# Performance work log

Measured on AMD Instinct MI355X. Metric: run time of the kernel, lower is better.

The kernel has to match this reference:

```python
import jax, jax.numpy as jnp
import numpy as np

POOL = 7          # output pooling resolution (Mask R-CNN box head)
IMG = 1024.0      # assumed input image size (boxes are normalized)
CANON = 224.0     # canonical ROI size for FPN level assignment


def _make_boxes(key, B, N):
    k1, k2, k3, k4 = jax.random.split(key, 4)
    y1 = jax.random.uniform(k1, (B, N)) * 0.7
    x1 = jax.random.uniform(k2, (B, N)) * 0.7
    h = jax.random.uniform(k3, (B, N)) * 0.28 + 0.01
    w = jax.random.uniform(k4, (B, N)) * 0.28 + 0.01
    return jnp.stack([y1, x1, jnp.minimum(y1 + h, 1.0), jnp.minimum(x1 + w, 1.0)], axis=-1)


def setup_inputs() -> dict:
    key = jax.random.key(0)
    k3, k4, k5, k6, kb = jax.random.split(key, 5)
    B, C, N = 2, 256, 1000
    return {
        "p3": jax.random.normal(k3, (B, 128, 128, C), jnp.float32),
        "p4": jax.random.normal(k4, (B, 64, 64, C), jnp.float32),
        "p5": jax.random.normal(k5, (B, 32, 32, C), jnp.float32),
        "p6": jax.random.normal(k6, (B, 16, 16, C), jnp.float32),
        "proposals": _make_boxes(kb, B, N),
    }


def _crop_resize(f, boxes):
    # f: [H, W, C]; boxes: [N, 4] normalized (y1, x1, y2, x2).
    # Matches tf.image.crop_and_resize bilinear sampling (crop_size > 1).
    H, W, _ = f.shape
    y1, x1, y2, x2 = boxes[:, 0], boxes[:, 1], boxes[:, 2], boxes[:, 3]
    t = jnp.arange(POOL, dtype=f.dtype) / (POOL - 1)          # [P]
    ys = (y1[:, None] + t[None, :] * (y2 - y1)[:, None]) * (H - 1)  # [N, P]
    xs = (x1[:, None] + t[None, :] * (x2 - x1)[:, None]) * (W - 1)  # [N, P]
    y0f = jnp.floor(ys); x0f = jnp.floor(xs)
    fy = ys - y0f; fx = xs - x0f                                # fractional parts
    y0 = jnp.clip(y0f.astype(jnp.int32), 0, H - 1)
    y1i = jnp.clip(y0 + 1, 0, H - 1)
    x0 = jnp.clip(x0f.astype(jnp.int32), 0, W - 1)
    x1i = jnp.clip(x0 + 1, 0, W - 1)
    # gather 4 corners: index broadcast [N,P,1] x [N,1,P] -> [N,P,P,C]
    v00 = f[y0[:, :, None], x0[:, None, :]]
    v01 = f[y0[:, :, None], x1i[:, None, :]]
    v10 = f[y1i[:, :, None], x0[:, None, :]]
    v11 = f[y1i[:, :, None], x1i[:, None, :]]
    wy = fy[:, :, None, None]; wx = fx[:, None, :, None]
    top = v00 + wx * (v01 - v00)
    bot = v10 + wx * (v11 - v10)
    return top + wy * (bot - top)                               # [N, P, P, C]


def reference(p3, p4, p5, p6, proposals):
    # proposals: [B, N, 4] normalized (y1, x1, y2, x2)
    h = proposals[..., 2] - proposals[..., 0]
    w = proposals[..., 3] - proposals[..., 1]
    # FPN level assignment (levels 3..6)
    roi_level = jnp.log2(jnp.sqrt(jnp.maximum(h * w, 0.0)) / (CANON / IMG) + 1e-8)
    lvl = jnp.clip(4 + jnp.round(roi_level).astype(jnp.int32), 3, 6)  # [B, N]
    B, N = lvl.shape
    C = p3.shape[-1]
    pooled = jnp.zeros((B, N, POOL, POOL, C), p3.dtype)
    for li, f in zip((3, 4, 5, 6), (p3, p4, p5, p6)):
        p = jax.vmap(_crop_resize)(f, proposals)                # [B, N, P, P, C]
        pooled = jnp.where((lvl == li)[:, :, None, None, None], p, pooled)
    return pooled
```

## Files before the change

### kernel.cpp

```cpp
#include <hip/hip_runtime.h>

#define POOL 7
#define NPTS 49

typedef float f4 __attribute__((ext_vector_type(4)));

__device__ __forceinline__ f4 ld4(const float* p) { return *(const f4*)p; }

__device__ __forceinline__ int roi_level(float dy, float dx) {
    const float rl = log2f(sqrtf(fmaxf(dy * dx, 0.0f)) / 0.21875f + 1e-8f);
    int lvl = 4 + (int)rintf(rl);
    return lvl < 3 ? 3 : (lvl > 6 ? 6 : lvl);
}

__device__ __forceinline__ int bucket_key(const float* props, int r, int N) {
    const f4 p = ld4(props + (size_t)r * 4);
    const int lvl = roi_level(p.z - p.x, p.w - p.y);
    const float yc = 0.5f * (p.x + p.z);
    int oct = (int)(yc * 8.0f);
    oct = oct < 0 ? 0 : (oct > 7 ? 7 : oct);
    int lg = lvl - 3; lg = lg < 0 ? 0 : (lg > 1 ? 1 : lg);
    const int b = r >= N ? 1 : 0;
    return ((b << 1) | lg) * 8 + oct;
}

__global__ __launch_bounds__(1024) void bucket_kernel(
    const float* __restrict__ props, int* __restrict__ order, int BN, int N)
{
    __shared__ int hist[32];
    __shared__ int offs[32];
    const int tid = threadIdx.x;
    if (tid < 32) hist[tid] = 0;
    __syncthreads();
    for (int r = tid; r < BN; r += 1024)
        atomicAdd(&hist[bucket_key(props, r, N)], 1);
    __syncthreads();
    if (tid == 0) {
        int acc = 0;
        for (int i = 0; i < 32; ++i) { offs[i] = acc; acc += hist[i]; }
    }
    __syncthreads();
    for (int r = tid; r < BN; r += 1024) {
        const int k = bucket_key(props, r, N);
        const int pos = atomicAdd(&offs[k], 1);
        order[pos] = r;
    }
}

__global__ __launch_bounds__(256) void roialign_kernel(
    const float* __restrict__ p3, const float* __restrict__ p4,
    const float* __restrict__ p5, const float* __restrict__ p6,
    const float* __restrict__ props, const int* __restrict__ order,
    float* __restrict__ out, int B, int N, int C, int nwg)
{
    const int s   = blockIdx.x;
    const int q   = nwg >> 3, rr = nwg & 7;
    const int xcd = s & 7, idx = s >> 3;
    const int s2  = (xcd < rr ? xcd * (q + 1) : rr * (q + 1) + (xcd - rr) * q) + idx;
    const int roi = order[s2];
    const int b   = roi >= N ? 1 : 0;

    const f4 pv = ld4(props + (size_t)roi * 4);
    const float y1 = pv.x, x1 = pv.y, y2 = pv.z, x2 = pv.w;
    const float dy = y2 - y1, dx = x2 - x1;

    const int lvl = roi_level(dy, dx);
    const float* f;
    int H;
    if      (lvl == 3) { f = p3; H = 128; }
    else if (lvl == 4) { f = p4; H = 64;  }
    else if (lvl == 5) { f = p5; H = 32;  }
    else               { f = p6; H = 16;  }
    const int W = H;
    const float hm1 = (float)(H - 1);
    const float* fb = f + (size_t)b * H * W * C;

    const int tid = threadIdx.x;
    const int pl  = tid >> 6;
    const int cg  = (tid & 63) << 2;

    const int obase = roi * NPTS * C + cg;

    auto calc = [&](int p, int& o00, int& o01, int& o10, int& o11,
                    float& fx, float& fy) {
        const int py = p / POOL;
        const int px = p - py * POOL;
        const float ys = (y1 + (float)py * (1.0f / (POOL - 1)) * dy) * hm1;
        const float xs = (x1 + (float)px * (1.0f / (POOL - 1)) * dx) * hm1;
        const float y0f = floorf(ys);
        const float x0f = floorf(xs);
        fy = ys - y0f;
        fx = xs - x0f;
        int yA = (int)y0f; yA = yA < 0 ? 0 : (yA > H - 1 ? H - 1 : yA);
        int yB = yA + 1;   yB = yB > H - 1 ? H - 1 : yB;
        int xA = (int)x0f; xA = xA < 0 ? 0 : (xA > W - 1 ? W - 1 : xA);
        int xB = xA + 1;   xB = xB > W - 1 ? W - 1 : xB;
        const int rA = yA * W, rB = yB * W;
        o00 = (rA + xA) * C + cg;
        o01 = (rA + xB) * C + cg;
        o10 = (rB + xA) * C + cg;
        o11 = (rB + xB) * C + cg;
    };

    #pragma unroll
    for (int p0 = 0; p0 < 48; p0 += 8) {
        const int pa = p0 + pl;
        const int pb = pa + 4;
        int a00, a01, a10, a11, b00, b01, b10, b11;
        float afx, afy, bfx, bfy;
        calc(pa, a00, a01, a10, a11, afx, afy);
        calc(pb, b00, b01, b10, b11, bfx, bfy);

        const f4 va00 = ld4(fb + a00), va01 = ld4(fb + a01);
        const f4 va10 = ld4(fb + a10), va11 = ld4(fb + a11);
        const f4 vb00 = ld4(fb + b00), vb01 = ld4(fb + b01);
        const f4 vb10 = ld4(fb + b10), vb11 = ld4(fb + b11);

        const f4 ta = va00 + afx * (va01 - va00);
        const f4 ba = va10 + afx * (va11 - va10);
        const f4 oa = ta + afy * (ba - ta);
        const f4 tb = vb00 + bfx * (vb01 - vb00);
        const f4 bb = vb10 + bfx * (vb11 - vb10);
        const f4 ob = tb + bfy * (bb - tb);

        __builtin_nontemporal_store(oa, (f4*)(out + obase + pa * C));
        __builtin_nontemporal_store(ob, (f4*)(out + obase + pb * C));
    }

    if (pl == 0) {
        int o00, o01, o10, o11;
        float fx, fy;
        calc(48, o00, o01, o10, o11, fx, fy);
        const f4 v00 = ld4(fb + o00), v01 = ld4(fb + o01);
        const f4 v10 = ld4(fb + o10), v11 = ld4(fb + o11);
        const f4 t  = v00 + fx * (v01 - v00);
        const f4 bo = v10 + fx * (v11 - v10);
        const f4 o  = t + fy * (bo - t);
        __builtin_nontemporal_store(o, (f4*)(out + obase + 48 * C));
    }
}

extern "C" void kernel_launch(void* const* d_in, const int* in_sizes, int n_in,
                              void* d_out, int out_size, void* d_ws, size_t ws_size,
                              hipStream_t stream) {
    (void)ws_size; (void)n_in; (void)out_size;

    const float* p3 = (const float*)d_in[0];
    const float* p4 = (const float*)d_in[1];
    const float* p5 = (const float*)d_in[2];
    const float* p6 = (const float*)d_in[3];
    const float* props = (const float*)d_in[4];
    float* out = (float*)d_out;
    int* order = (int*)d_ws;

    const int B = 2;
    const int N = in_sizes[4] / (B * 4);
    const int C = in_sizes[0] / (B * 128 * 128);
    const int BN = B * N;

    bucket_kernel<<<1, 1024, 0, stream>>>(props, order, BN, N);
    roialign_kernel<<<BN, 256, 0, stream>>>(p3, p4, p5, p6, props, order,
                                            out, B, N, C, BN);
}
```

Before: 32.89 us.

## Refine ROI bucketing and switch RoIAlign to persistent per-XCD grid

The bucket kernel now sorts ROIs by batch, coarse level and 64 y-center bins instead of 8, and caches each ROI's key in shared memory so it is computed only once. The RoIAlign kernel moves from one block per ROI to a fixed grid of 1024 persistent blocks. Each block strides through a contiguous per-XCD range of the sorted order, and launch bounds request 4 blocks per CU. The goal is better L2 locality of feature-map reads within each XCD and lower block launch overhead. The cost is less parallel slack and possible load imbalance across blocks. The keys array is sized 2048, which only holds for BN up to 2048.

```diff
diff --git a/kernel.cpp b/kernel.cpp
--- a/kernel.cpp
+++ b/kernel.cpp
@@ -2,6 +2,7 @@
 
 #define POOL 7
 #define NPTS 49
+#define NBUCKET 256
 
 typedef float f4 __attribute__((ext_vector_type(4)));
 
@@ -13,130 +14,134 @@
     return lvl < 3 ? 3 : (lvl > 6 ? 6 : lvl);
 }
 
-__device__ __forceinline__ int bucket_key(const float* props, int r, int N) {
-    const f4 p = ld4(props + (size_t)r * 4);
-    const int lvl = roi_level(p.z - p.x, p.w - p.y);
-    const float yc = 0.5f * (p.x + p.z);
-    int oct = (int)(yc * 8.0f);
-    oct = oct < 0 ? 0 : (oct > 7 ? 7 : oct);
-    int lg = lvl - 3; lg = lg < 0 ? 0 : (lg > 1 ? 1 : lg);
-    const int b = r >= N ? 1 : 0;
-    return ((b << 1) | lg) * 8 + oct;
-}
-
 __global__ __launch_bounds__(1024) void bucket_kernel(
     const float* __restrict__ props, int* __restrict__ order, int BN, int N)
 {
-    __shared__ int hist[32];
-    __shared__ int offs[32];
+    __shared__ unsigned char keys[2048];
+    __shared__ int hist[NBUCKET];
+    __shared__ int offs[NBUCKET];
     const int tid = threadIdx.x;
-    if (tid < 32) hist[tid] = 0;
+    if (tid < NBUCKET) hist[tid] = 0;
     __syncthreads();
-    for (int r = tid; r < BN; r += 1024)
-        atomicAdd(&hist[bucket_key(props, r, N)], 1);
+    for (int r = tid; r < BN; r += 1024) {
+        const f4 p = ld4(props + (size_t)r * 4);
+        const int lvl = roi_level(p.z - p.x, p.w - p.y);
+        int lg = lvl - 3; lg = lg < 0 ? 0 : (lg > 1 ? 1 : lg);
+        const float yc = 0.5f * (p.x + p.z);
+        int yq = (int)(yc * 64.0f);
+        yq = yq < 0 ? 0 : (yq > 63 ? 63 : yq);
+        const int b = r >= N ? 1 : 0;
+        const int k = (b << 7) | (lg << 6) | yq;
+        keys[r] = (unsigned char)k;
+        atomicAdd(&hist[k], 1);
+    }
     __syncthreads();
     if (tid == 0) {
         int acc = 0;
-        for (int i = 0; i < 32; ++i) { offs[i] = acc; acc += hist[i]; }
+        for (int i = 0; i < NBUCKET; ++i) { offs[i] = acc; acc += hist[i]; }
     }
     __syncthreads();
     for (int r = tid; r < BN; r += 1024) {
-        const int k = bucket_key(props, r, N);
-        const int pos = atomicAdd(&offs[k], 1);
+        const int pos = atomicAdd(&offs[keys[r]], 1);
         order[pos] = r;
     }
 }
 
-__global__ __launch_bounds__(256) void roialign_kernel(
+__global__ __launch_bounds__(256, 4) void roialign_kernel(
     const float* __restrict__ p3, const float* __restrict__ p4,
     const float* __restrict__ p5, const float* __restrict__ p6,
     const float* __restrict__ props, const int* __restrict__ order,
-    float* __restrict__ out, int B, int N, int C, int nwg)
+    float* __restrict__ out, int B, int N, int C, int BN)
 {
-    const int s   = blockIdx.x;
-    const int q   = nwg >> 3, rr = nwg & 7;
-    const int xcd = s & 7, idx = s >> 3;
-    const int s2  = (xcd < rr ? xcd * (q + 1) : rr * (q + 1) + (xcd - rr) * q) + idx;
-    const int roi = order[s2];
-    const int b   = roi >= N ? 1 : 0;
-
-    const f4 pv = ld4(props + (size_t)roi * 4);
-    const float y1 = pv.x, x1 = pv.y, y2 = pv.z, x2 = pv.w;
-    const float dy = y2 - y1, dx = x2 - x1;
-
-    const int lvl = roi_level(dy, dx);
-    const float* f;
-    int H;
-    if      (lvl == 3) { f = p3; H = 128; }
-    else if (lvl == 4) { f = p4; H = 64;  }
-    else if (lvl == 5) { f = p5; H = 32;  }
-    else               { f = p6; H = 16;  }
-    const int W = H;
-    const float hm1 = (float)(H - 1);
-    const float* fb = f + (size_t)b * H * W * C;
+    const int bid = blockIdx.x;
+    const int xcd = bid & 7;
+    const int j   = bid >> 3;
+    const int q = BN >> 3, rr = BN & 7;
+    const int cs = xcd < rr ? xcd * (q + 1) : rr * (q + 1) + (xcd - rr) * q;
+    const int ce = cs + q + (xcd < rr ? 1 : 0);
 
     const int tid = threadIdx.x;
     const int pl  = tid >> 6;
     const int cg  = (tid & 63) << 2;
 
-    const int obase = roi * NPTS * C + cg;
+    for (int s = cs + j; s < ce; s += 128) {
+        const int roi = order[s];
+        const int b   = roi >= N ? 1 : 0;
 
-    auto calc = [&](int p, int& o00, int& o01, int& o10, int& o11,
-                    float& fx, float& fy) {
-        const int py = p / POOL;
-        const int px = p - py * POOL;
-        const float ys = (y1 + (float)py * (1.0f / (POOL - 1)) * dy) * hm1;
-        const float xs = (x1 + (float)px * (1.0f / (POOL - 1)) * dx) * hm1;
-        const float y0f = floorf(ys);
-        const float x0f = floorf(xs);
-        fy = ys - y0f;
-        fx = xs - x0f;
-        int yA = (int)y0f; yA = yA < 0 ? 0 : (yA > H - 1 ? H - 1 : yA);
-        int yB = yA + 1;   yB = yB > H - 1 ? H - 1 : yB;
-        int xA = (int)x0f; xA = xA < 0 ? 0 : (xA > W - 1 ? W - 1 : xA);
-        int xB = xA + 1;   xB = xB > W - 1 ? W - 1 : xB;
-        const int rA = yA * W, rB = yB * W;
-        o00 = (rA + xA) * C + cg;
-        o01 = (rA + xB) * C + cg;
-        o10 = (rB + xA) * C + cg;
-        o11 = (rB + xB) * C + cg;
-    };
+        const f4 pv = ld4(props + (size_t)roi * 4);
+        const float y1 = pv.x, x1 = pv.y, y2 = pv.z, x2 = pv.w;
+        const float dy = y2 - y1, dx = x2 - x1;
 
-    #pragma unroll
-    for (int p0 = 0; p0 < 48; p0 += 8) {
-        const int pa = p0 + pl;
-        const int pb = pa + 4;
-        int a00, a01, a10, a11, b00, b01, b10, b11;
-        float afx, afy, bfx, bfy;
-        calc(pa, a00, a01, a10, a11, afx, afy);
-        calc(pb, b00, b01, b10, b11, bfx, bfy);
+        const int lvl = roi_level(dy, dx);
+        const float* f;
+        int H;
+        if      (lvl == 3) { f = p3; H = 128; }
+        else if (lvl == 4) { f = p4; H = 64;  }
+        else if (lvl == 5) { f = p5; H = 32;  }
+        else               { f = p6; H = 16;  }
+        const int W = H;
+        const float hm1 = (float)(H - 1);
+        const float* fb = f + (size_t)b * H * W * C;
 
-        const f4 va00 = ld4(fb + a00), va01 = ld4(fb + a01);
-        const f4 va10 = ld4(fb + a10), va11 = ld4(fb + a11);
-        const f4 vb00 = ld4(fb + b00), vb01 = ld4(fb + b01);
-        const f4 vb10 = ld4(fb + b10), vb11 = ld4(fb + b11);
+        const int obase = roi * NPTS * C + cg;
 
-        const f4 ta = va00 + afx * (va01 - va00);
-        const f4 ba = va10 + afx * (va11 - va10);
-        const f4 oa = ta + afy * (ba - ta);
-        const f4 tb = vb00 + bfx * (vb01 - vb00);
-        const f4 bb = vb10 + bfx * (vb11 - vb10);
-        const f4 ob = tb + bfy * (bb - tb);
+        auto calc = [&](int p, int& o00, int& o01, int& o10, int& o11,
+                        float& fx, float& fy) {
+            const int py = p / POOL;
+            const int px = p - py * POOL;
+            const float ys = (y1 + (float)py * (1.0f / (POOL - 1)) * dy) * hm1;
+            const float xs = (x1 + (float)px * (1.0f / (POOL - 1)) * dx) * hm1;
+            const float y0f = floorf(ys);
+            const float x0f = floorf(xs);
+            fy = ys - y0f;
+            fx = xs - x0f;
+            int yA = (int)y0f; yA = yA < 0 ? 0 : (yA > H - 1 ? H - 1 : yA);
+            int yB = yA + 1;   yB = yB > H - 1 ? H - 1 : yB;
+            int xA = (int)x0f; xA = xA < 0 ? 0 : (xA > W - 1 ? W - 1 : xA);
+            int xB = xA + 1;   xB = xB > W - 1 ? W - 1 : xB;
+            const int rA = yA * W, rB = yB * W;
+            o00 = (rA + xA) * C + cg;
+            o01 = (rA + xB) * C + cg;
+            o10 = (rB + xA) * C + cg;
+            o11 = (rB + xB) * C + cg;
+        };
 
-        __builtin_nontemporal_store(oa, (f4*)(out + obase + pa * C));
-        __builtin_nontemporal_store(ob, (f4*)(out + obase + pb * C));
-    }
+        #pragma unroll
+        for (int p0 = 0; p0 < 48; p0 += 8) {
+            const int pa = p0 + pl;
+            const int pb = pa + 4;
+            int a00, a01, a10, a11, b00, b01, b10, b11;
+            float afx, afy, bfx, bfy;
+            calc(pa, a00, a01, a10, a11, afx, afy);
+            calc(pb, b00, b01, b10, b11, bfx, bfy);
 
-    if (pl == 0) {
-        int o00, o01, o10, o11;
-        float fx, fy;
-        calc(48, o00, o01, o10, o11, fx, fy);
-        const f4 v00 = ld4(fb + o00), v01 = ld4(fb + o01);
-        const f4 v10 = ld4(fb + o10), v11 = ld4(fb + o11);
-        const f4 t  = v00 + fx * (v01 - v00);
-        const f4 bo = v10 + fx * (v11 - v10);
-        const f4 o  = t + fy * (bo - t);
-        __builtin_nontemporal_store(o, (f4*)(out + obase + 48 * C));
+            const f4 va00 = ld4(fb + a00), va01 = ld4(fb + a01);
+            const f4 va10 = ld4(fb + a10), va11 = ld4(fb + a11);
+            const f4 vb00 = ld4(fb + b00), vb01 = ld4(fb + b01);
+            const f4 vb10 = ld4(fb + b10), vb11 = ld4(fb + b11);
+
+            const f4 ta = va00 + afx * (va01 - va00);
+            const f4 ba = va10 + afx * (va11 - va10);
+            const f4 oa = ta + afy * (ba - ta);
+            const f4 tb = vb00 + bfx * (vb01 - vb00);
+            const f4 bb = vb10 + bfx * (vb11 - vb10);
+            const f4 ob = tb + bfy * (bb - tb);
+
+            __builtin_nontemporal_store(oa, (f4*)(out + obase + pa * C));
+            __builtin_nontemporal_store(ob, (f4*)(out + obase + pb * C));
+        }
+
+        if (pl == 0) {
+            int o00, o01, o10, o11;
+            float fx, fy;
+            calc(48, o00, o01, o10, o11, fx, fy);
+            const f4 v00 = ld4(fb + o00), v01 = ld4(fb + o01);
+            const f4 v10 = ld4(fb + o10), v11 = ld4(fb + o11);
+            const f4 t  = v00 + fx * (v01 - v00);
+            const f4 bo = v10 + fx * (v11 - v10);
+            const f4 o  = t + fy * (bo - t);
+            __builtin_nontemporal_store(o, (f4*)(out + obase + 48 * C));
+        }
     }
 }
 
@@ -159,6 +164,6 @@
     const int BN = B * N;
 
     bucket_kernel<<<1, 1024, 0, stream>>>(props, order, BN, N);
-    roialign_kernel<<<BN, 256, 0, stream>>>(p3, p4, p5, p6, props, order,
-                                            out, B, N, C, BN);
+    roialign_kernel<<<1024, 256, 0, stream>>>(p3, p4, p5, p6, props, order,
+                                              out, B, N, C, BN);
 }
```

New measurement: 35.47 us. 7.8% more time.
